# Performance work log

Measured on AMD Instinct MI355X. Metric: run time of the kernel, lower is better.

The kernel has to match this reference:

```python
import jax, jax.numpy as jnp
import numpy as np

D_MODEL = 1024
N_HEADS = 16
HDIM = D_MODEL // N_HEADS
IMP_EPS = 1e-6


def setup_inputs() -> dict:
    key = jax.random.key(0)
    ks = jax.random.split(key, 7)
    B, T_q, T_kv, N_s = 2, 2048, 256, 16
    scale = 1.0 / np.sqrt(D_MODEL)
    return {
        "query": jax.random.normal(ks[0], (B, T_q, D_MODEL), dtype=jnp.float32),
        "key_value": jax.random.normal(ks[1], (B, T_kv, N_s, D_MODEL), dtype=jnp.float32),
        "imp_weights": jax.random.uniform(ks[2], (B, N_s), dtype=jnp.float32),
        "W_q": jax.random.normal(ks[3], (D_MODEL, D_MODEL), dtype=jnp.float32) * scale,
        "W_k": jax.random.normal(ks[4], (D_MODEL, D_MODEL), dtype=jnp.float32) * scale,
        "W_v": jax.random.normal(ks[5], (D_MODEL, D_MODEL), dtype=jnp.float32) * scale,
        "W_o": jax.random.normal(ks[6], (D_MODEL, D_MODEL), dtype=jnp.float32) * scale,
    }


def _split_heads(x):
    # [B, T, D] -> [B, h, T, d]
    B, T, _ = x.shape
    return x.reshape(B, T, N_HEADS, HDIM).transpose(0, 2, 1, 3)


def reference(query, key_value, imp_weights, W_q, W_k, W_v, W_o):
    # CAU_MultiheadCrossAttention.forward with 4D key_value (sensor axis).
    B, T_q, D = query.shape
    _, T_kv, N_s, _ = key_value.shape
    kv = key_value.reshape(B, T_kv * N_s, D)  # flatten sensor axis into source length S

    qh = _split_heads(query @ W_q.T)   # [B,h,T_q,d]  (nn.Linear: x @ W.T)
    kh = _split_heads(kv @ W_k.T)      # [B,h,S,d]
    vh = _split_heads(kv @ W_v.T)      # [B,h,S,d]

    # importance: [B,N_s] -> tiled over T_kv -> [B, S], log-clamped additive mask
    imp_full = jnp.broadcast_to(imp_weights[:, None, :], (B, T_kv, N_s)).reshape(B, T_kv * N_s)
    log_imp = jnp.log(jnp.clip(imp_full, IMP_EPS, None)).astype(qh.dtype)  # [B,S]

    scores = jnp.einsum("bhqd,bhkd->bhqk", qh, kh) / np.sqrt(HDIM).astype(np.float32)
    scores = scores + log_imp[:, None, None, :]
    attn = jax.nn.softmax(scores, axis=-1)
    y = jnp.einsum("bhqk,bhkd->bhqd", attn, vh)  # [B,h,T_q,d]

    y = y.transpose(0, 2, 1, 3).reshape(B, T_q, D)  # merge heads
    return y @ W_o.T
```

## Files before the change

kernel.cpp:

```cpp
#include <hip/hip_runtime.h>
#include <hip/hip_bf16.h>

typedef __bf16    bf16x8_t __attribute__((ext_vector_type(8)));
typedef __bf16    bf16x4_t __attribute__((ext_vector_type(4)));
typedef float     f32x4_t  __attribute__((ext_vector_type(4)));
typedef _Float16  f16x8_t  __attribute__((ext_vector_type(8)));

static __device__ __forceinline__ f32x4_t mfma16(bf16x8_t a, bf16x8_t b, f32x4_t c) {
    return __builtin_amdgcn_mfma_f32_16x16x32_bf16(a, b, c, 0, 0, 0);
}

static __device__ __forceinline__ float redsum16(float v) {
#pragma unroll
    for (int off = 1; off < 16; off <<= 1) v += __shfl_xor(v, off);
    return v;
}

static __device__ __forceinline__ void async16(const __bf16* g, __bf16* l) {
    __builtin_amdgcn_global_load_lds(
        (const __attribute__((address_space(1))) unsigned int*)g,
        (__attribute__((address_space(3))) unsigned int*)l, 16, 0, 0);
}

__global__ __launch_bounds__(256) void f2b_multi(const float* __restrict__ q,
                                                 const float* __restrict__ kv,
                                                 const float* __restrict__ wq,
                                                 const float* __restrict__ wk,
                                                 const float* __restrict__ wv,
                                                 const float* __restrict__ wo,
                                                 __bf16* __restrict__ qb,
                                                 __bf16* __restrict__ kvb,
                                                 __bf16* __restrict__ wqb,
                                                 __bf16* __restrict__ wkvb,
                                                 __bf16* __restrict__ wob,
                                                 float qscale) {
    int i = blockIdx.x * 256 + threadIdx.x;
    const float* src; __bf16* dst; int base; float scale = 1.0f;
    if (i < 1048576)      { src = q;  dst = qb;   base = 0; }
    else if (i < 3145728) { src = kv; dst = kvb;  base = 1048576; }
    else if (i < 3407872) { src = wq; dst = wqb;  base = 3145728; scale = qscale; }
    else if (i < 3670016) { src = wk; dst = wkvb; base = 3407872; }
    else if (i < 3932160) { src = wv; dst = wkvb + 1048576; base = 3670016; }
    else                  { src = wo; dst = wob;  base = 3932160; }
    int j = i - base;
    float4 v = reinterpret_cast<const float4*>(src)[j];
    bf16x4_t o;
    o[0] = (__bf16)(v.x * scale); o[1] = (__bf16)(v.y * scale);
    o[2] = (__bf16)(v.z * scale); o[3] = (__bf16)(v.w * scale);
    reinterpret_cast<bf16x4_t*>(dst)[j] = o;
}

__global__ __launch_bounds__(256) void proj_kernel(const __bf16* __restrict__ qb,
                                                   const __bf16* __restrict__ wqb,
                                                   const __bf16* __restrict__ kvb,
                                                   const __bf16* __restrict__ wkvb,
                                                   __bf16* __restrict__ Qp,
                                                   __bf16* __restrict__ Khd,
                                                   __bf16* __restrict__ Vhd,
                                                   const float* __restrict__ imp) {
    __shared__ __bf16 As[128 * 32];
    __shared__ __bf16 Bs[128 * 32];
    __shared__ __bf16 Es[2][4096];

    const int gid = blockIdx.x;
    const __bf16 *A, *B;
    long m0, n0;
    int mode;
    if (gid < 256) {
        m0 = (long)(gid >> 3) * 128; n0 = (long)(gid & 7) * 128;
        A = qb; B = wqb; mode = 0;
    } else {
        int g2 = gid - 256;
        m0 = (long)(g2 >> 4) * 128; n0 = (long)(g2 & 15) * 128;
        A = kvb; B = wkvb; mode = (n0 < 1024) ? 1 : 2;
    }

    const int t    = threadIdx.x;
    const int w    = t >> 6;
    const int lane = t & 63;
    const int quad = lane >> 4;
    const int mn   = lane & 15;
    const int wm   = (w & 1) * 64;
    const int wn   = (w >> 1) * 64;

    const int  srow = t >> 2;
    const int  scol = (t & 3) * 8;
    const __bf16* gA = A + (m0 + srow) * 1024 + scol;
    const __bf16* gB = B + (n0 + srow) * 1024 + scol;

    f32x4_t acc[4][4];
#pragma unroll
    for (int i = 0; i < 4; i++)
#pragma unroll
        for (int j = 0; j < 4; j++) acc[i][j] = (f32x4_t){0.f, 0.f, 0.f, 0.f};

    for (int k0 = 0; k0 < 1024; k0 += 32) {
        __syncthreads();
        async16(gA + k0,              &As[t * 8]);
        async16(gA + 64 * 1024 + k0,  &As[2048 + t * 8]);
        async16(gB + k0,              &Bs[t * 8]);
        async16(gB + 64 * 1024 + k0,  &Bs[2048 + t * 8]);
        __syncthreads();

        bf16x8_t af[4], bf[4];
#pragma unroll
        for (int i = 0; i < 4; i++)
            af[i] = *(const bf16x8_t*)&As[(wm + i * 16 + mn) * 32 + quad * 8];
#pragma unroll
        for (int j = 0; j < 4; j++)
            bf[j] = *(const bf16x8_t*)&Bs[(wn + j * 16 + mn) * 32 + quad * 8];
#pragma unroll
        for (int i = 0; i < 4; i++)
#pragma unroll
            for (int j = 0; j < 4; j++) acc[i][j] = mfma16(af[i], bf[j], acc[i][j]);
    }

    __syncthreads();
    __bf16* stg = (w == 0) ? As : (w == 1) ? Bs : Es[w - 2];

    if (mode != 2) {
#pragma unroll
        for (int i = 0; i < 4; i++)
#pragma unroll
            for (int j = 0; j < 4; j++)
#pragma unroll
                for (int r = 0; r < 4; r++) {
                    int sl = i * 16 + quad * 4 + r;
                    int d  = j * 16 + mn;
                    stg[sl * 64 + (((d >> 3) ^ (sl & 7)) * 8) + (d & 7)] =
                        (__bf16)acc[i][j][r];
                }
    } else {
        const int b_ = (int)((m0 + wm) >> 12);
#pragma unroll
        for (int r = 0; r < 4; r++) {
            float scl = fmaxf(imp[b_ * 16 + quad * 4 + r], 1e-6f);
#pragma unroll
            for (int j = 0; j < 4; j++) {
                bf16x4_t pk;
#pragma unroll
                for (int i = 0; i < 4; i++) pk[i] = (__bf16)(acc[i][j][r] * scl);
                int d  = j * 16 + mn;
                int p0 = (quad * 4 + r) * 4;
                *(bf16x4_t*)&stg[d * 64 + (((p0 >> 3) ^ (d & 7)) * 8) + (p0 & 7)] = pk;
            }
        }
    }

    if (mode == 0) {
        __bf16* Cg = Qp + (m0 + wm) * 1024 + (n0 + wn);
#pragma unroll
        for (int it = 0; it < 8; it++) {
            int rowL = it * 8 + (lane >> 3);
            int cb   = lane & 7;
            bf16x8_t vv = *(const bf16x8_t*)&stg[rowL * 64 + ((cb ^ (rowL & 7)) * 8)];
            *(bf16x8_t*)&Cg[(long)rowL * 1024 + cb * 8] = vv;
        }
    } else {
        const int b_    = (int)((m0 + wm) >> 12);
        const int sbase = (int)((m0 + wm) & 4095);
        __bf16* dst;
        if (mode == 1) {
            int h_ = (int)((n0 + wn) >> 6);
            dst = Khd + (long)(b_ * 16 + h_) * 262144 + (long)sbase * 64;
        } else {
            int h_ = (int)((n0 + wn) >> 6) - 16;
            dst = Vhd + (long)(b_ * 16 + h_) * 262144 + (long)(sbase >> 6) * 4096;
        }
#pragma unroll
        for (int it = 0; it < 8; it++) {
            int rowL = it * 8 + (lane >> 3);
            int cb   = lane & 7;
            bf16x8_t vv = *(const bf16x8_t*)&stg[rowL * 64 + ((cb ^ (rowL & 7)) * 8)];
            *(bf16x8_t*)&dst[rowL * 64 + cb * 8] = vv;
        }
    }
}

__global__ __launch_bounds__(256, 4) void attn_kernel(const __bf16* __restrict__ Qp,
                                                      const __bf16* __restrict__ Kh,
                                                      const __bf16* __restrict__ Vh,
                                                      const float* __restrict__ imp,
                                                      _Float16* __restrict__ Op,
                                                      float* __restrict__ Lp) {
    const int gid = blockIdx.x;
    const int qt  = (gid >> 3) & 15;
    const int sp  = (gid >> 7) & 1;
    const int bh  = ((gid >> 8) << 3) | (gid & 7);
    const int b   = bh >> 4;
    const int h   = bh & 15;
    const int t    = threadIdx.x;
    const int w    = t >> 6;
    const int lane = t & 63;
    const int quad = lane >> 4;
    const int mn   = lane & 15;

    __shared__ __bf16 Ks[64 * 64];
    __shared__ __bf16 Vs[64 * 64];
    __shared__ __bf16 Ps[4][32][72];

    const long qrow0 = (long)b * 2048 + qt * 128 + w * 32;
    const __bf16* Kb = Kh + (long)bh * 262144;
    const __bf16* Vb = Vh + (long)bh * 262144;

    const int r8 = lane >> 3;
    const int cs = (lane & 7) ^ r8;
    const int srcoff0 = (0 * 4 + w) * 512 + r8 * 64 + cs * 8;
    const int srcoff1 = (1 * 4 + w) * 512 + r8 * 64 + cs * 8;
    __bf16* ldsK0 = Ks + (0 * 4 + w) * 512;
    __bf16* ldsK1 = Ks + (1 * 4 + w) * 512;
    __bf16* ldsV0 = Vs + (0 * 4 + w) * 512;
    __bf16* ldsV1 = Vs + (1 * 4 + w) * 512;

    bf16x8_t aq[2][2];
#pragma unroll
    for (int rt = 0; rt < 2; rt++)
#pragma unroll
        for (int x = 0; x < 2; x++)
            aq[rt][x] = *(const bf16x8_t*)&Qp[(qrow0 + rt * 16 + mn) * 1024 + h * 64 + x * 32 + quad * 8];

    const float impc = fmaxf(imp[b * 16 + mn], 1e-6f);

    float lpart[2][4];
    f32x4_t o[2][4];
#pragma unroll
    for (int rt = 0; rt < 2; rt++)
#pragma unroll
        for (int r = 0; r < 4; r++) lpart[rt][r] = 0.f;
#pragma unroll
    for (int rt = 0; rt < 2; rt++)
#pragma unroll
        for (int dt = 0; dt < 4; dt++) o[rt][dt] = (f32x4_t){0.f, 0.f, 0.f, 0.f};

    for (int st = sp * 32; st < sp * 32 + 32; st++) {
        const long kbase = (long)st * 4096;
        __syncthreads();
        async16(Kb + kbase + srcoff0, ldsK0);
        async16(Kb + kbase + srcoff1, ldsK1);
        async16(Vb + kbase + srcoff0, ldsV0);
        async16(Vb + kbase + srcoff1, ldsV1);
        __syncthreads();

        f32x4_t sc[2][4];
        {
            bf16x8_t bk0[4], bk1[4];
#pragma unroll
            for (int ct = 0; ct < 4; ct++) {
                int s  = ct * 16 + mn;
                int c0 = (quad ^ (s & 7)) * 8;
                bk0[ct] = *(const bf16x8_t*)&Ks[s * 64 + c0];
                bk1[ct] = *(const bf16x8_t*)&Ks[s * 64 + (c0 ^ 32)];
            }
#pragma unroll
            for (int rt = 0; rt < 2; rt++) {
#pragma unroll
                for (int ct = 0; ct < 4; ct++) sc[rt][ct] = (f32x4_t){0.f, 0.f, 0.f, 0.f};
#pragma unroll
                for (int ct = 0; ct < 4; ct++) {
                    sc[rt][ct] = mfma16(aq[rt][0], bk0[ct], sc[rt][ct]);
                    sc[rt][ct] = mfma16(aq[rt][1], bk1[ct], sc[rt][ct]);
                }
            }
        }

#pragma unroll
        for (int rt = 0; rt < 2; rt++)
#pragma unroll
            for (int r = 0; r < 4; r++) {
                float p0 = __builtin_amdgcn_exp2f(sc[rt][0][r]);
                float p1 = __builtin_amdgcn_exp2f(sc[rt][1][r]);
                float p2 = __builtin_amdgcn_exp2f(sc[rt][2][r]);
                float p3 = __builtin_amdgcn_exp2f(sc[rt][3][r]);
                lpart[rt][r] += (p0 + p1) + (p2 + p3);
                bf16x4_t pk;
                pk[0] = (__bf16)p0; pk[1] = (__bf16)p1;
                pk[2] = (__bf16)p2; pk[3] = (__bf16)p3;
                *(bf16x4_t*)&Ps[w][rt * 16 + quad * 4 + r][mn * 4] = pk;
            }

        {
            bf16x8_t bv0[4], bv1[4];
#pragma unroll
            for (int dt = 0; dt < 4; dt++) {
                int d  = dt * 16 + mn;
                int c0 = (quad ^ (d & 7)) * 8;
                bv0[dt] = *(const bf16x8_t*)&Vs[d * 64 + c0];
                bv1[dt] = *(const bf16x8_t*)&Vs[d * 64 + (c0 ^ 32)];
            }
#pragma unroll
            for (int rt = 0; rt < 2; rt++) {
                bf16x8_t ap0 = *(const bf16x8_t*)&Ps[w][rt * 16 + mn][quad * 8];
                bf16x8_t ap1 = *(const bf16x8_t*)&Ps[w][rt * 16 + mn][32 + quad * 8];
#pragma unroll
                for (int dt = 0; dt < 4; dt++) {
                    o[rt][dt] = mfma16(ap0, bv0[dt], o[rt][dt]);
                    o[rt][dt] = mfma16(ap1, bv1[dt], o[rt][dt]);
                }
            }
        }
    }

#pragma unroll
    for (int rt = 0; rt < 2; rt++)
#pragma unroll
        for (int r = 0; r < 4; r++) {
            float l = redsum16(lpart[rt][r] * impc);
            long row = qrow0 + rt * 16 + quad * 4 + r;
            if (mn == 0) Lp[((long)sp * 4096 + row) * 16 + h] = l;
#pragma unroll
            for (int dt = 0; dt < 4; dt++)
                Op[((long)sp * 4096 + row) * 1024 + h * 64 + dt * 16 + mn] =
                    (_Float16)o[rt][dt][r];
        }
}

__global__ __launch_bounds__(256) void combine_kernel(const _Float16* __restrict__ Op,
                                                      const float* __restrict__ Lp,
                                                      __bf16* __restrict__ Y) {
    int tid = blockIdx.x * 256 + threadIdx.x;
    int row = tid >> 7;
    int cg  = tid & 127;
    int h   = cg >> 3;
    f16x8_t o0 = *(const f16x8_t*)&Op[(long)row * 1024 + cg * 8];
    f16x8_t o1 = *(const f16x8_t*)&Op[(long)(4096 + row) * 1024 + cg * 8];
    float inv = 1.0f / (Lp[row * 16 + h] + Lp[(4096 + row) * 16 + h]);
    bf16x8_t y;
#pragma unroll
    for (int j = 0; j < 8; j++) y[j] = (__bf16)(((float)o0[j] + (float)o1[j]) * inv);
    *(bf16x8_t*)&Y[(long)row * 1024 + cg * 8] = y;
}

__global__ __launch_bounds__(256) void gemm_out_kernel(const __bf16* __restrict__ A,
                                                       const __bf16* __restrict__ B,
                                                       float* __restrict__ P) {
    __shared__ __bf16 As[128 * 32];
    __shared__ __bf16 Bs[128 * 32];

    const int  kh = blockIdx.x >> 3;
    const long n0 = (long)(blockIdx.x & 7) * 128;
    const long m0 = (long)blockIdx.y * 128;
    const int  kb = kh * 512;
    float* C = P + (long)kh * 4194304;

    const int t    = threadIdx.x;
    const int w    = t >> 6;
    const int lane = t & 63;
    const int quad = lane >> 4;
    const int mn   = lane & 15;
    const int wm   = (w & 1) * 64;
    const int wn   = (w >> 1) * 64;

    const int  srow = t >> 2;
    const int  scol = (t & 3) * 8;
    const __bf16* gA = A + (m0 + srow) * 1024 + kb + scol;
    const __bf16* gB = B + (n0 + srow) * 1024 + kb + scol;

    f32x4_t acc[4][4];
#pragma unroll
    for (int i = 0; i < 4; i++)
#pragma unroll
        for (int j = 0; j < 4; j++) acc[i][j] = (f32x4_t){0.f, 0.f, 0.f, 0.f};

    for (int k0 = 0; k0 < 512; k0 += 32) {
        __syncthreads();
        async16(gA + k0,             &As[t * 8]);
        async16(gA + 64 * 1024 + k0, &As[2048 + t * 8]);
        async16(gB + k0,             &Bs[t * 8]);
        async16(gB + 64 * 1024 + k0, &Bs[2048 + t * 8]);
        __syncthreads();

        bf16x8_t af[4], bf[4];
#pragma unroll
        for (int i = 0; i < 4; i++)
            af[i] = *(const bf16x8_t*)&As[(wm + i * 16 + mn) * 32 + quad * 8];
#pragma unroll
        for (int j = 0; j < 4; j++)
            bf[j] = *(const bf16x8_t*)&Bs[(wn + j * 16 + mn) * 32 + quad * 8];
#pragma unroll
        for (int i = 0; i < 4; i++)
#pragma unroll
            for (int j = 0; j < 4; j++) acc[i][j] = mfma16(af[i], bf[j], acc[i][j]);
    }

#pragma unroll
    for (int i = 0; i < 4; i++)
#pragma unroll
        for (int j = 0; j < 4; j++)
#pragma unroll
            for (int r = 0; r < 4; r++) {
                long row = m0 + wm + i * 16 + quad * 4 + r;
                long col = n0 + wn + j * 16 + mn;
                C[row * 1024 + col] = acc[i][j][r];
            }
}

__global__ __launch_bounds__(256) void combine2_kernel(const float* __restrict__ P0,
                                                       const float* __restrict__ P1,
                                                       float* __restrict__ out) {
    int i = blockIdx.x * 256 + threadIdx.x;
    float4 a = reinterpret_cast<const float4*>(P0)[i];
    float4 b = reinterpret_cast<const float4*>(P1)[i];
    float4 c; c.x = a.x + b.x; c.y = a.y + b.y; c.z = a.z + b.z; c.w = a.w + b.w;
    reinterpret_cast<float4*>(out)[i] = c;
}

extern "C" void kernel_launch(void* const* d_in, const int* in_sizes, int n_in,
                              void* d_out, int out_size, void* d_ws, size_t ws_size,
                              hipStream_t stream) {
    const float* q_f  = (const float*)d_in[0];
    const float* kv_f = (const float*)d_in[1];
    const float* imp  = (const float*)d_in[2];
    const float* wq_f = (const float*)d_in[3];
    const float* wk_f = (const float*)d_in[4];
    const float* wv_f = (const float*)d_in[5];
    const float* wo_f = (const float*)d_in[6];

    char* ws = (char*)d_ws;
    const size_t MB = 1ull << 20;
    __bf16*   qb    = (__bf16*)(ws + 0);
    __bf16*   kvb   = (__bf16*)(ws + 8 * MB);
    __bf16*   wqb   = (__bf16*)(ws + 24 * MB);
    __bf16*   wkvb  = (__bf16*)(ws + 26 * MB);
    _Float16* Opart = (_Float16*)(ws + 0);
    float*    Lpart = (float*)(ws + 16 * MB);
    __bf16*   Yb    = (__bf16*)(ws + 17 * MB);
    __bf16*   wob   = (__bf16*)(ws + 30 * MB);
    __bf16*   Qp    = (__bf16*)(ws + 32 * MB);
    __bf16*   Khd   = (__bf16*)(ws + 40 * MB);
    __bf16*   Vhd   = (__bf16*)(ws + 56 * MB);
    float*    Gp    = (float*)(ws + 40 * MB);

    const float QSCALE = 0.125f * 1.4426950408889634f;

    f2b_multi<<<16384, 256, 0, stream>>>(q_f, kv_f, wq_f, wk_f, wv_f, wo_f,
                                         qb, kvb, wqb, wkvb, wob, QSCALE);

    proj_kernel<<<1280, 256, 0, stream>>>(qb, wqb, kvb, wkvb, Qp, Khd, Vhd, imp);

    attn_kernel<<<1024, 256, 0, stream>>>(Qp, Khd, Vhd, imp, Opart, Lpart);
    combine_kernel<<<2048, 256, 0, stream>>>(Opart, Lpart, Yb);

    gemm_out_kernel<<<dim3(16, 32), 256, 0, stream>>>(Yb, wob, Gp);
    combine2_kernel<<<4096, 256, 0, stream>>>(Gp, Gp + 4194304, (float*)d_out);
}
```

Baseline: 294.4 us.

## Double-buffer K tiles in LDS and load V straight from global

Result: slower. 343.9 us (+16.8%).

```diff
diff --git a/kernel.cpp b/kernel.cpp
--- a/kernel.cpp
+++ b/kernel.cpp
@@ -195,8 +195,7 @@
     const int quad = lane >> 4;
     const int mn   = lane & 15;
 
-    __shared__ __bf16 Ks[64 * 64];
-    __shared__ __bf16 Vs[64 * 64];
+    __shared__ __bf16 Ks[2][64 * 64];
     __shared__ __bf16 Ps[4][32][72];
 
     const long qrow0 = (long)b * 2048 + qt * 128 + w * 32;
@@ -207,10 +206,6 @@
     const int cs = (lane & 7) ^ r8;
     const int srcoff0 = (0 * 4 + w) * 512 + r8 * 64 + cs * 8;
     const int srcoff1 = (1 * 4 + w) * 512 + r8 * 64 + cs * 8;
-    __bf16* ldsK0 = Ks + (0 * 4 + w) * 512;
-    __bf16* ldsK1 = Ks + (1 * 4 + w) * 512;
-    __bf16* ldsV0 = Vs + (0 * 4 + w) * 512;
-    __bf16* ldsV1 = Vs + (1 * 4 + w) * 512;
 
     bf16x8_t aq[2][2];
 #pragma unroll
@@ -232,35 +227,49 @@
 #pragma unroll
         for (int dt = 0; dt < 4; dt++) o[rt][dt] = (f32x4_t){0.f, 0.f, 0.f, 0.f};
 
-    for (int st = sp * 32; st < sp * 32 + 32; st++) {
-        const long kbase = (long)st * 4096;
-        __syncthreads();
-        async16(Kb + kbase + srcoff0, ldsK0);
-        async16(Kb + kbase + srcoff1, ldsK1);
-        async16(Vb + kbase + srcoff0, ldsV0);
-        async16(Vb + kbase + srcoff1, ldsV1);
-        __syncthreads();
+    const int st0 = sp * 32;
+
+    async16(Kb + (long)st0 * 4096 + srcoff0, &Ks[0][(0 * 4 + w) * 512]);
+    async16(Kb + (long)st0 * 4096 + srcoff1, &Ks[0][(1 * 4 + w) * 512]);
+    __syncthreads();
+
+    for (int it = 0; it < 32; ++it) {
+        const int st  = st0 + it;
+        const int cur = it & 1;
+        const __bf16* Kc = &Ks[cur][0];
 
         f32x4_t sc[2][4];
+#pragma unroll
+        for (int rt = 0; rt < 2; rt++)
+#pragma unroll
+            for (int ct = 0; ct < 4; ct++) sc[rt][ct] = (f32x4_t){0.f, 0.f, 0.f, 0.f};
+#pragma unroll
+        for (int ct = 0; ct < 4; ct++) {
+            int s  = ct * 16 + mn;
+            int c0 = (quad ^ (s & 7)) * 8;
+            bf16x8_t bk0 = *(const bf16x8_t*)&Kc[s * 64 + c0];
+            bf16x8_t bk1 = *(const bf16x8_t*)&Kc[s * 64 + (c0 ^ 32)];
+#pragma unroll
+            for (int rt = 0; rt < 2; rt++) {
+                sc[rt][ct] = mfma16(aq[rt][0], bk0, sc[rt][ct]);
+                sc[rt][ct] = mfma16(aq[rt][1], bk1, sc[rt][ct]);
+            }
+        }
+
+        bf16x8_t bv0[4], bv1[4];
         {
-            bf16x8_t bk0[4], bk1[4];
-#pragma unroll
-            for (int ct = 0; ct < 4; ct++) {
-                int s  = ct * 16 + mn;
-                int c0 = (quad ^ (s & 7)) * 8;
-                bk0[ct] = *(const bf16x8_t*)&Ks[s * 64 + c0];
-                bk1[ct] = *(const bf16x8_t*)&Ks[s * 64 + (c0 ^ 32)];
-            }
-#pragma unroll
-            for (int rt = 0; rt < 2; rt++) {
-#pragma unroll
-                for (int ct = 0; ct < 4; ct++) sc[rt][ct] = (f32x4_t){0.f, 0.f, 0.f, 0.f};
-#pragma unroll
-                for (int ct = 0; ct < 4; ct++) {
-                    sc[rt][ct] = mfma16(aq[rt][0], bk0[ct], sc[rt][ct]);
-                    sc[rt][ct] = mfma16(aq[rt][1], bk1[ct], sc[rt][ct]);
-                }
-            }
+            const __bf16* vb = Vb + (long)st * 4096 + mn * 64 + quad * 8;
+#pragma unroll
+            for (int dt = 0; dt < 4; dt++) {
+                bv0[dt] = *(const bf16x8_t*)&vb[dt * 1024];
+                bv1[dt] = *(const bf16x8_t*)&vb[dt * 1024 + 32];
+            }
+        }
+
+        {
+            __bf16* kn = &Ks[cur ^ 1][0];
+            async16(Kb + (long)(st + 1) * 4096 + srcoff0, kn + (0 * 4 + w) * 512);
+            async16(Kb + (long)(st + 1) * 4096 + srcoff1, kn + (1 * 4 + w) * 512);
         }
 
 #pragma unroll
@@ -278,26 +287,18 @@
                 *(bf16x4_t*)&Ps[w][rt * 16 + quad * 4 + r][mn * 4] = pk;
             }
 
-        {
-            bf16x8_t bv0[4], bv1[4];
+#pragma unroll
+        for (int rt = 0; rt < 2; rt++) {
+            bf16x8_t ap0 = *(const bf16x8_t*)&Ps[w][rt * 16 + mn][quad * 8];
+            bf16x8_t ap1 = *(const bf16x8_t*)&Ps[w][rt * 16 + mn][32 + quad * 8];
 #pragma unroll
             for (int dt = 0; dt < 4; dt++) {
-                int d  = dt * 16 + mn;
-                int c0 = (quad ^ (d & 7)) * 8;
-                bv0[dt] = *(const bf16x8_t*)&Vs[d * 64 + c0];
-                bv1[dt] = *(const bf16x8_t*)&Vs[d * 64 + (c0 ^ 32)];
-            }
-#pragma unroll
-            for (int rt = 0; rt < 2; rt++) {
-                bf16x8_t ap0 = *(const bf16x8_t*)&Ps[w][rt * 16 + mn][quad * 8];
-                bf16x8_t ap1 = *(const bf16x8_t*)&Ps[w][rt * 16 + mn][32 + quad * 8];
-#pragma unroll
-                for (int dt = 0; dt < 4; dt++) {
-                    o[rt][dt] = mfma16(ap0, bv0[dt], o[rt][dt]);
-                    o[rt][dt] = mfma16(ap1, bv1[dt], o[rt][dt]);
-                }
-            }
-        }
+                o[rt][dt] = mfma16(ap0, bv0[dt], o[rt][dt]);
+                o[rt][dt] = mfma16(ap1, bv1[dt], o[rt][dt]);
+            }
+        }
+
+        __syncthreads();
     }
 
 #pragma unroll
```
